# Performance work log

Measured on AMD Instinct MI355X. Metric: run time of the kernel, lower is better.

The kernel has to match this reference:

```python
import jax, jax.numpy as jnp
import numpy as np
import math

B, S, D = 16, 512, 1024
H, L = 16, 4
DH = D // H
EPS = 1e-5


def _layernorm(x, w, b):
    mu = jnp.mean(x, axis=-1, keepdims=True)
    var = jnp.mean(jnp.square(x - mu), axis=-1, keepdims=True)
    return (x - mu) / jnp.sqrt(var + EPS) * w + b


def _pos_encoding(s, d):
    pos = jnp.arange(s, dtype=jnp.float32)[:, None]                      # [s,1]
    div = jnp.exp(jnp.arange(0, d, 2, dtype=jnp.float32) * (-math.log(10000.0) / d))
    ang = pos * div[None, :]                                             # [s,d/2]
    return jnp.stack([jnp.sin(ang), jnp.cos(ang)], axis=-1).reshape(s, d)  # interleave sin/cos


def _attention_layer(x, Wq, bq, Wv, bv, Wo, bo, gamma, ln_w, ln_b, mask):
    bs, s, d = x.shape
    # q_linear == k_linear (kq_same=True)
    q = (x @ Wq.T + bq).reshape(bs, s, H, DH).transpose(0, 2, 1, 3)      # [b,h,s,dh]
    k = q
    v = (x @ Wv.T + bv).reshape(bs, s, H, DH).transpose(0, 2, 1, 3)

    scores = jnp.einsum('bhqd,bhkd->bhqk', q, k) / math.sqrt(DH)         # [b,h,s,s]

    # distance-decay modulation (dist_scores is detached in the original)
    p = jax.nn.softmax(jnp.where(mask, scores, -1e32), axis=-1)
    distcum = jnp.cumsum(p, axis=-1)
    disttot = jnp.sum(p, axis=-1, keepdims=True)
    idx = jnp.arange(s, dtype=jnp.float32)
    pos_eff = jnp.abs(idx[None, :] - idx[:, None])[None, None, :, :]     # |i-j|
    dist = jnp.sqrt(jnp.maximum((disttot - distcum) * pos_eff, 0.0))
    dist = jax.lax.stop_gradient(dist)

    g = -jnp.abs(gamma)[None, :, None, None]                             # [1,h,1,1]
    total_effect = jnp.clip(jnp.exp(dist * g), 1e-5, 1e5)
    scores = scores * total_effect

    scores = jnp.where(mask, scores, -1e32)
    attn = jax.nn.softmax(scores, axis=-1)
    attn = jnp.where(mask, attn, 0.0)

    # maxout=True (peek_cur=False): clamp(1/max, max=5)
    scale = jnp.minimum(1.0 / jnp.max(attn, axis=-1, keepdims=True), 5.0)
    attn = attn * scale

    out = jnp.einsum('bhqk,bhkd->bhqd', attn, v)                         # [b,h,s,dh]
    out = out.transpose(0, 2, 1, 3).reshape(bs, s, d)
    out = out @ Wo.T + bo

    # eval mode: dropout = identity; residual + layernorm
    return _layernorm(x + out, ln_w, ln_b), attn


def reference(x, lens, Wq, bq, Wv, bv, Wo, bo, gammas, ln_w, ln_b, fln_w, fln_b):
    del lens  # only used in training-mode random masking
    s = x.shape[1]
    q = x + _pos_encoding(s, D)[None, :, :]
    mask = jnp.tril(jnp.ones((s, s), dtype=bool), -1)[None, None, :, :]  # peek_cur=False
    scores = None
    for l in range(L):
        q, scores = _attention_layer(q, Wq[l], bq[l], Wv[l], bv[l], Wo[l], bo[l],
                                     gammas[l], ln_w[l], ln_b[l], mask)
    return _layernorm(q, fln_w, fln_b), scores


def setup_inputs() -> dict:
    key = jax.random.key(0)
    ks = jax.random.split(key, 8)
    wscale = 1.0 / math.sqrt(D)
    return {
        'x': jax.random.normal(ks[0], (B, S, D), dtype=jnp.float32),
        'lens': jax.random.randint(ks[1], (B,), 1, S),
        'Wq': jax.random.normal(ks[2], (L, D, D), dtype=jnp.float32) * wscale,
        'bq': jnp.zeros((L, D), dtype=jnp.float32),
        'Wv': jax.random.normal(ks[3], (L, D, D), dtype=jnp.float32) * wscale,
        'bv': jnp.zeros((L, D), dtype=jnp.float32),
        'Wo': jax.random.normal(ks[4], (L, D, D), dtype=jnp.float32) * wscale,
        'bo': jnp.zeros((L, D), dtype=jnp.float32),
        'gammas': jax.random.uniform(ks[5], (L, H), dtype=jnp.float32, minval=-1.7, maxval=1.7),
        'ln_w': jnp.ones((L, D), dtype=jnp.float32),
        'ln_b': jnp.zeros((L, D), dtype=jnp.float32),
        'fln_w': jnp.ones((D,), dtype=jnp.float32),
        'fln_b': jnp.zeros((D,), dtype=jnp.float32),
    }
```

## Files before the change

### kernel.cpp

```cpp
#include <hip/hip_runtime.h>
#include <hip/hip_bf16.h>

#define BB 16
#define SS 512
#define DD 1024
#define HH 16
#define LL 4
#define DHH 64
#define GK 1024

typedef __attribute__((ext_vector_type(8))) short short8;
typedef __attribute__((ext_vector_type(4))) float f32x4;
typedef __attribute__((ext_vector_type(8))) _Float16 half8;

__device__ __forceinline__ unsigned short f2bf(float f) {
  union { float f; unsigned int u; } v; v.f = f;
  unsigned int r = v.u + 0x7FFFu + ((v.u >> 16) & 1u);
  return (unsigned short)(r >> 16);
}
__device__ __forceinline__ float bf2f(unsigned short u) {
  union { unsigned int i; float f; } v; v.i = ((unsigned)u) << 16; return v.f;
}

__device__ __forceinline__ float wave_max(float v) {
#pragma unroll
  for (int off = 32; off > 0; off >>= 1) v = fmaxf(v, __shfl_xor(v, off));
  return v;
}
__device__ __forceinline__ float wave_sum(float v) {
#pragma unroll
  for (int off = 32; off > 0; off >>= 1) v += __shfl_xor(v, off);
  return v;
}
__device__ __forceinline__ float half_max(float v) {
#pragma unroll
  for (int off = 16; off > 0; off >>= 1) v = fmaxf(v, __shfl_xor(v, off));
  return v;
}
__device__ __forceinline__ float half_sum(float v) {
#pragma unroll
  for (int off = 16; off > 0; off >>= 1) v += __shfl_xor(v, off);
  return v;
}

__device__ __forceinline__ void gl16(const void* g, void* l) {
  __builtin_amdgcn_global_load_lds(
      (const __attribute__((address_space(1))) unsigned int*)(uintptr_t)g,
      (__attribute__((address_space(3))) unsigned int*)(unsigned int)(uintptr_t)l,
      16, 0, 0);
}

__global__ __launch_bounds__(256) void k_w2bf_all(
    const float* __restrict__ wq, const float* __restrict__ wv,
    const float* __restrict__ wo, unsigned short* __restrict__ oqv,
    unsigned short* __restrict__ oo) {
  size_t i4 = ((size_t)blockIdx.x * 256 + threadIdx.x) * 4;
  const size_t QV = (size_t)2 * LL * DD * DD;
  const float* src;
  unsigned short* dst;
  if (i4 < QV) {
    size_t l = i4 >> 21;
    size_t r = i4 & ((1u << 21) - 1);
    src = (r < (1u << 20)) ? wq + (l << 20) + r
                           : wv + (l << 20) + (r - (1u << 20));
    dst = oqv + i4;
  } else {
    size_t j = i4 - QV;
    src = wo + j;
    dst = oo + j;
  }
  float4 v = *(const float4*)src;
  uint2 pk;
  pk.x = (unsigned)f2bf(v.x) | ((unsigned)f2bf(v.y) << 16);
  pk.y = (unsigned)f2bf(v.z) | ((unsigned)f2bf(v.w) << 16);
  *(uint2*)dst = pk;
}

__global__ __launch_bounds__(256) void k_add_pe(const float* __restrict__ x,
                                                unsigned short* __restrict__ outb) {
  size_t i4 = ((size_t)blockIdx.x * 256 + threadIdx.x) * 4;
  int d0 = (int)(i4 & (DD - 1));
  int s = (int)((i4 >> 10) & (SS - 1));
  float4 xv = *(const float4*)(x + i4);
  int ip0 = d0 >> 1;
  float f0 = __expf((float)ip0 * -0.017988946039016f);
  float f1 = __expf((float)(ip0 + 1) * -0.017988946039016f);
  float s0v, c0v, s1v, c1v;
  __sincosf((float)s * f0, &s0v, &c0v);
  __sincosf((float)s * f1, &s1v, &c1v);
  float o0 = xv.x + s0v, o1 = xv.y + c0v, o2 = xv.z + s1v, o3 = xv.w + c1v;
  uint2 pk;
  pk.x = (unsigned)f2bf(o0) | ((unsigned)f2bf(o1) << 16);
  pk.y = (unsigned)f2bf(o2) | ((unsigned)f2bf(o3) << 16);
  *(uint2*)(outb + i4) = pk;
}

template <int MODE>
__global__ __launch_bounds__(256) void k_gemm(
    const unsigned short* __restrict__ A, const unsigned short* __restrict__ W,
    const float* __restrict__ bias, const float* __restrict__ bias2,
    void* __restrict__ out, void* __restrict__ out2) {
  __shared__ unsigned short As[2][128 * 32];
  __shared__ unsigned short Bs[2][128 * 32];
  const int tid = threadIdx.x;
  const int lane = tid & 63;
  const int w = tid >> 6;
  const int wr = w >> 1, wc = w & 1;
  const int fr = lane & 15, fq = lane >> 4;

  int bid = blockIdx.x;
  const int cpx = gridDim.x >> 3;
  bid = (bid & 7) * cpx + (bid >> 3);
  const int bm = (bid & 63) * 128;
  const int bn = (bid >> 6) * 128;

  f32x4 acc[4][4] = {};

  const unsigned short* ga = A + (size_t)(bm + w * 16 + (lane >> 2)) * GK + (lane & 3) * 8;
  const unsigned short* gb = W + (size_t)(bn + w * 16 + (lane >> 2)) * GK + (lane & 3) * 8;

  auto STAGE = [&](int buf, int k0) {
    unsigned short* la = As[buf] + w * 512;
    unsigned short* lb = Bs[buf] + w * 512;
    gl16(ga + k0, la);
    gl16(ga + 64 * GK + k0, la + 2048);
    gl16(gb + k0, lb);
    gl16(gb + 64 * GK + k0, lb + 2048);
  };

  STAGE(0, 0);
  __syncthreads();
  int cur = 0;
  for (int k0 = 0; k0 < GK; k0 += 32) {
    if (k0 + 32 < GK) STAGE(cur ^ 1, k0 + 32);
    short8 af[4], bf[4];
#pragma unroll
    for (int m = 0; m < 4; ++m)
      af[m] = *(const short8*)(As[cur] + (wr * 64 + m * 16 + fr) * 32 + fq * 8);
#pragma unroll
    for (int n = 0; n < 4; ++n)
      bf[n] = *(const short8*)(Bs[cur] + (wc * 64 + n * 16 + fr) * 32 + fq * 8);
#pragma unroll
    for (int m = 0; m < 4; ++m)
#pragma unroll
      for (int n = 0; n < 4; ++n)
        acc[m][n] = __builtin_amdgcn_mfma_f32_16x16x32_bf16(af[m], bf[n], acc[m][n], 0, 0, 0);
    __syncthreads();
    cur ^= 1;
  }

#pragma unroll
  for (int m = 0; m < 4; ++m) {
    const int row0 = bm + wr * 64 + m * 16 + fq * 4;
#pragma unroll
    for (int n = 0; n < 4; ++n) {
      const int col = bn + wc * 64 + n * 16 + fr;
      if constexpr (MODE == 0) {
        const float bsv = bias[col];
        unsigned short* o = (unsigned short*)out;
#pragma unroll
        for (int r = 0; r < 4; ++r)
          o[(size_t)(row0 + r) * DD + col] = f2bf(acc[m][n][r] + bsv);
      } else {
        if (col < DD) {
          const float bsv = bias[col];
          unsigned short* o = (unsigned short*)out;
#pragma unroll
          for (int r = 0; r < 4; ++r)
            o[(size_t)(row0 + r) * DD + col] = f2bf(acc[m][n][r] + bsv);
        } else {
          const int c2 = col - DD;
          const float bsv = bias2[c2];
          unsigned short* o = (unsigned short*)out2;
          const int bi = row0 >> 9, si = row0 & (SS - 1);
          uint2 pk;
          pk.x = (unsigned)f2bf(acc[m][n][0] + bsv) | ((unsigned)f2bf(acc[m][n][1] + bsv) << 16);
          pk.y = (unsigned)f2bf(acc[m][n][2] + bsv) | ((unsigned)f2bf(acc[m][n][3] + bsv) << 16);
          *(uint2*)(o + ((size_t)bi * DD + c2) * SS + si) = pk;
        }
      }
    }
  }
}

__global__ __launch_bounds__(512) void k_attn(
    const unsigned short* __restrict__ Q, const unsigned short* __restrict__ Vt,
    const float* __restrict__ gam, unsigned short* __restrict__ AO,
    float* __restrict__ scores_out) {
  __shared__ _Float16 sc_s[64][520];
  __shared__ unsigned short KV[64][72];

  const int tid = threadIdx.x;
  const int lane = tid & 63;
  const int w = tid >> 6;
  const int wr = w & 3;
  const int wc = w >> 2;
  const int fr = lane & 15, fq = lane >> 4;

  const int itile = 7 - (blockIdx.x >> 8);
  const int bh = blockIdx.x & 255;
  const int b = bh >> 4;
  const int h = bh & 15;
  const int i0 = itile * 64;
  const int njt = itile + 1;
  const int jcap = njt * 64;

  const unsigned short* Qb = Q + (size_t)b * SS * DD + h * DHH;
  const unsigned short* Vtb = Vt + ((size_t)b * DD + h * DHH) * SS;
  const float gneg = -fabsf(gam[h]);

  const int srow = tid >> 3;
  const int sdb = (tid & 7) * 8;

  const unsigned short* qrow = Qb + (size_t)(i0 + wr * 16 + fr) * DD;
  short8 a0 = *(const short8*)(qrow + fq * 8);
  short8 a1 = *(const short8*)(qrow + 32 + fq * 8);

  short8 kreg = *(const short8*)(Qb + (size_t)srow * DD + sdb);
  for (int jt = 0; jt < njt; ++jt) {
    *(short8*)&KV[srow][sdb] = kreg;
    const unsigned short* nsrc = (jt + 1 < njt)
        ? Qb + (size_t)((jt + 1) * 64 + srow) * DD + sdb
        : Vtb + (size_t)srow * SS + sdb;
    kreg = *(const short8*)nsrc;
    __syncthreads();

    short8 b00 = *(const short8*)&KV[wc * 32 + fr][fq * 8];
    short8 b01 = *(const short8*)&KV[wc * 32 + fr][32 + fq * 8];
    short8 b10 = *(const short8*)&KV[wc * 32 + 16 + fr][fq * 8];
    short8 b11 = *(const short8*)&KV[wc * 32 + 16 + fr][32 + fq * 8];
    f32x4 s0 = {}, s1 = {};
    __builtin_amdgcn_s_setprio(1);
    s0 = __builtin_amdgcn_mfma_f32_16x16x32_bf16(a0, b00, s0, 0, 0, 0);
    s0 = __builtin_amdgcn_mfma_f32_16x16x32_bf16(a1, b01, s0, 0, 0, 0);
    s1 = __builtin_amdgcn_mfma_f32_16x16x32_bf16(a0, b10, s1, 0, 0, 0);
    s1 = __builtin_amdgcn_mfma_f32_16x16x32_bf16(a1, b11, s1, 0, 0, 0);
    __builtin_amdgcn_s_setprio(0);

#pragma unroll
    for (int n = 0; n < 2; ++n) {
      const int j = jt * 64 + wc * 32 + n * 16 + fr;
#pragma unroll
      for (int r = 0; r < 4; ++r) {
        const int row = wr * 16 + fq * 4 + r;
        const float val = (n ? s1[r] : s0[r]) * 0.125f;
        sc_s[row][j] = (j < i0 + row) ? (_Float16)val : (_Float16)(-65504.0f);
      }
    }
    __syncthreads();
  }
  *(short8*)&KV[srow][sdb] = kreg;

  if (itile >= 4) {
    const int jb = lane << 3;
#pragma unroll 2
    for (int q = 0; q < 8; ++q) {
      const int r_i = w * 8 + q;
      const int gi = i0 + r_i;
      half8 hv = *(const half8*)(&sc_s[r_i][0] + jb);
      float sc[8];
#pragma unroll
      for (int c = 0; c < 8; ++c) sc[c] = (float)hv[c];
#pragma unroll
      for (int c = 0; c < 8; ++c)
        if (jb + c >= jcap) sc[c] = -1e30f;

      float p[8];
      float lsum = 0.0f;
#pragma unroll
      for (int c = 0; c < 8; ++c) {
        p[c] = __expf(sc[c]);
        lsum += p[c];
      }

      float xs = lsum;
#pragma unroll
      for (int off = 1; off < 64; off <<= 1) {
        float y = __shfl_up(xs, off);
        if (lane >= off) xs += y;
      }
      const float tot = __shfl(xs, 63);
      const float inv = 1.0f / tot;
      float run = xs - lsum;

      float s2[8];
      float m2l = -3e38f;
#pragma unroll
      for (int c = 0; c < 8; ++c) {
        run += p[c];
        float cum = run * inv;
        float dist = sqrtf(fmaxf((1.0f - cum) * (float)(gi - (jb + c)), 0.0f));
        float te = __expf(gneg * dist);
        te = fminf(fmaxf(te, 1e-5f), 1e5f);
        s2[c] = sc[c] * te;
        m2l = fmaxf(m2l, s2[c]);
      }
      float e[8];
      float ls2 = 0.0f;
#pragma unroll
      for (int c = 0; c < 8; ++c) {
        e[c] = __expf(s2[c]);
        ls2 += e[c];
      }
      const float m2 = wave_max(m2l);
      const float tot2 = wave_sum(ls2);
      const float rr = tot2 * __expf(-m2);
      const float mult = fminf(rr, 5.0f) / tot2;

      float av[8];
#pragma unroll
      for (int c = 0; c < 8; ++c) av[c] = (gi == 0) ? 0.0f : e[c] * mult;

      if (scores_out) {
        float* so = scores_out + ((size_t)(b * HH + h) * SS + gi) * SS + jb;
        *(float4*)(so) = make_float4(av[0], av[1], av[2], av[3]);
        *(float4*)(so + 4) = make_float4(av[4], av[5], av[6], av[7]);
      }

      short8 pk;
#pragma unroll
      for (int c = 0; c < 8; ++c) pk[c] = (short)f2bf(av[c]);
      *(short8*)((unsigned short*)&sc_s[r_i][0] + jb) = pk;
    }
  } else {
    const int half = lane >> 5;
    const int ll = lane & 31;
    const int jb = ll << 3;
    for (int q = 0; q < 4; ++q) {
      const int r_i = w * 8 + q * 2 + half;
      const int gi = i0 + r_i;
      half8 hv = *(const half8*)(&sc_s[r_i][0] + jb);
      float sc[8];
#pragma unroll
      for (int c = 0; c < 8; ++c) sc[c] = (float)hv[c];
#pragma unroll
      for (int c = 0; c < 8; ++c)
        if (jb + c >= jcap) sc[c] = -1e30f;

      float p[8];
      float lsum = 0.0f;
#pragma unroll
      for (int c = 0; c < 8; ++c) {
        p[c] = __expf(sc[c]);
        lsum += p[c];
      }

      float xs = lsum;
#pragma unroll
      for (int off = 1; off < 32; off <<= 1) {
        float y = __shfl_up(xs, off, 32);
        if (ll >= off) xs += y;
      }
      const float tot = __shfl(xs, 31, 32);
      const float inv = 1.0f / tot;
      float run = xs - lsum;

      float s2[8];
      float m2l = -3e38f;
#pragma unroll
      for (int c = 0; c < 8; ++c) {
        run += p[c];
        float cum = run * inv;
        float dist = sqrtf(fmaxf((1.0f - cum) * (float)(gi - (jb + c)), 0.0f));
        float te = __expf(gneg * dist);
        te = fminf(fmaxf(te, 1e-5f), 1e5f);
        s2[c] = sc[c] * te;
        m2l = fmaxf(m2l, s2[c]);
      }
      float e[8];
      float ls2 = 0.0f;
#pragma unroll
      for (int c = 0; c < 8; ++c) {
        e[c] = __expf(s2[c]);
        ls2 += e[c];
      }
      const float m2 = half_max(m2l);
      const float tot2 = half_sum(ls2);
      const float rr = tot2 * __expf(-m2);
      const float mult = fminf(rr, 5.0f) / tot2;

      float av[8];
#pragma unroll
      for (int c = 0; c < 8; ++c) av[c] = (gi == 0) ? 0.0f : e[c] * mult;

      if (scores_out) {
        float* so = scores_out + ((size_t)(b * HH + h) * SS + gi) * SS + jb;
        *(float4*)(so) = make_float4(av[0], av[1], av[2], av[3]);
        *(float4*)(so + 4) = make_float4(av[4], av[5], av[6], av[7]);
        *(float4*)(so + 256) = make_float4(0.f, 0.f, 0.f, 0.f);
        *(float4*)(so + 260) = make_float4(0.f, 0.f, 0.f, 0.f);
      }

      short8 pk;
#pragma unroll
      for (int c = 0; c < 8; ++c) pk[c] = (short)f2bf(av[c]);
      *(short8*)((unsigned short*)&sc_s[r_i][0] + jb) = pk;
    }
  }
  __syncthreads();

  short8 vreg;
  if (njt > 1) vreg = *(const short8*)(Vtb + (size_t)srow * SS + 64 + sdb);
  f32x4 o0 = {}, o1 = {};
  for (int jt = 0; jt < njt; ++jt) {
    const unsigned short* arow = (const unsigned short*)&sc_s[wr * 16 + fr][0];
    short8 pa0 = *(const short8*)(arow + jt * 64 + fq * 8);
    short8 pa1 = *(const short8*)(arow + jt * 64 + 32 + fq * 8);
    short8 c00 = *(const short8*)&KV[wc * 32 + fr][fq * 8];
    short8 c01 = *(const short8*)&KV[wc * 32 + fr][32 + fq * 8];
    short8 c10 = *(const short8*)&KV[wc * 32 + 16 + fr][fq * 8];
    short8 c11 = *(const short8*)&KV[wc * 32 + 16 + fr][32 + fq * 8];
    __builtin_amdgcn_s_setprio(1);
    o0 = __builtin_amdgcn_mfma_f32_16x16x32_bf16(pa0, c00, o0, 0, 0, 0);
    o0 = __builtin_amdgcn_mfma_f32_16x16x32_bf16(pa1, c01, o0, 0, 0, 0);
    o1 = __builtin_amdgcn_mfma_f32_16x16x32_bf16(pa0, c10, o1, 0, 0, 0);
    o1 = __builtin_amdgcn_mfma_f32_16x16x32_bf16(pa1, c11, o1, 0, 0, 0);
    __builtin_amdgcn_s_setprio(0);
    __syncthreads();
    if (jt + 1 < njt) {
      *(short8*)&KV[srow][sdb] = vreg;
      if (jt + 2 < njt) vreg = *(const short8*)(Vtb + (size_t)srow * SS + (jt + 2) * 64 + sdb);
      __syncthreads();
    }
  }

#pragma unroll
  for (int n = 0; n < 2; ++n) {
    const int d = h * DHH + wc * 32 + n * 16 + fr;
#pragma unroll
    for (int r = 0; r < 4; ++r) {
      const int row = i0 + wr * 16 + fq * 4 + r;
      AO[((size_t)b * SS + row) * DD + d] = f2bf(n ? o1[r] : o0[r]);
    }
  }
}

__global__ __launch_bounds__(256) void k_res_ln(
    const unsigned short* __restrict__ x, const unsigned short* __restrict__ r,
    const float* __restrict__ w, const float* __restrict__ b,
    unsigned short* __restrict__ outb, float* __restrict__ outf) {
  __shared__ float red[4];
  const int row = blockIdx.x;
  const int tid = threadIdx.x;
  const int lane = tid & 63, wv = tid >> 6;
  uint2 xa = ((const uint2*)(x + (size_t)row * DD))[tid];
  float y0 = bf2f((unsigned short)xa.x);
  float y1 = bf2f((unsigned short)(xa.x >> 16));
  float y2 = bf2f((unsigned short)xa.y);
  float y3 = bf2f((unsigned short)(xa.y >> 16));
  if (r) {
    uint2 ra = ((const uint2*)(r + (size_t)row * DD))[tid];
    y0 += bf2f((unsigned short)ra.x);
    y1 += bf2f((unsigned short)(ra.x >> 16));
    y2 += bf2f((unsigned short)ra.y);
    y3 += bf2f((unsigned short)(ra.y >> 16));
  }
  float s = y0 + y1 + y2 + y3;
  s = wave_sum(s);
  if (lane == 0) red[wv] = s;
  __syncthreads();
  float mean = (red[0] + red[1] + red[2] + red[3]) * (1.0f / DD);
  __syncthreads();
  float d0 = y0 - mean, d1 = y1 - mean, d2 = y2 - mean, d3 = y3 - mean;
  float s2 = d0 * d0 + d1 * d1 + d2 * d2 + d3 * d3;
  s2 = wave_sum(s2);
  if (lane == 0) red[wv] = s2;
  __syncthreads();
  float var = (red[0] + red[1] + red[2] + red[3]) * (1.0f / DD);
  float rstd = rsqrtf(var + 1e-5f);
  float4 ww = ((const float4*)w)[tid];
  float4 bb = ((const float4*)b)[tid];
  float o0 = d0 * rstd * ww.x + bb.x;
  float o1 = d1 * rstd * ww.y + bb.y;
  float o2 = d2 * rstd * ww.z + bb.z;
  float o3 = d3 * rstd * ww.w + bb.w;
  if (outf) {
    ((float4*)(outf + (size_t)row * DD))[tid] = make_float4(o0, o1, o2, o3);
  } else {
    uint2 pk;
    pk.x = (unsigned)f2bf(o0) | ((unsigned)f2bf(o1) << 16);
    pk.y = (unsigned)f2bf(o2) | ((unsigned)f2bf(o3) << 16);
    ((uint2*)(outb + (size_t)row * DD))[tid] = pk;
  }
}

extern "C" void kernel_launch(void* const* d_in, const int* in_sizes, int n_in,
                              void* d_out, int out_size, void* d_ws, size_t ws_size,
                              hipStream_t stream) {
  (void)in_sizes; (void)n_in; (void)out_size; (void)ws_size;
  const float* x = (const float*)d_in[0];
  const float* Wq = (const float*)d_in[2];
  const float* bq = (const float*)d_in[3];
  const float* Wv = (const float*)d_in[4];
  const float* bv = (const float*)d_in[5];
  const float* Wo = (const float*)d_in[6];
  const float* bo = (const float*)d_in[7];
  const float* gam = (const float*)d_in[8];
  const float* lnw = (const float*)d_in[9];
  const float* lnb = (const float*)d_in[10];
  const float* flnw = (const float*)d_in[11];
  const float* flnb = (const float*)d_in[12];

  float* out0 = (float*)d_out;
  float* scores = out0 + (size_t)BB * SS * DD;
  const size_t BUF = (size_t)BB * SS * DD;
  const size_t WSZ = (size_t)LL * DD * DD;
  const size_t BHSS = (size_t)BB * HH * SS * SS;

  unsigned short* us = (unsigned short*)d_ws;
  unsigned short* Abf0 = us;
  unsigned short* Abf1 = us + BUF;
  unsigned short* Qbf = us + 2 * BUF;
  unsigned short* VtB = us + 3 * BUF;
  unsigned short* AObf = us + 4 * BUF;
  unsigned short* Pb = us + 5 * BUF;
  unsigned short* Wob = us + 6 * BUF;
  unsigned short* Wqvb = (unsigned short*)scores + (2 * BHSS - 2 * WSZ);

  const int M = BB * SS;

  k_w2bf_all<<<dim3(3 * WSZ / 1024), 256, 0, stream>>>(Wq, Wv, Wo, Wqvb, Wob);
  k_add_pe<<<dim3(BUF / 1024), 256, 0, stream>>>(x, Abf0);

  unsigned short* Acur = Abf0;
  unsigned short* Anx = Abf1;
  for (int l = 0; l < LL; ++l) {
    float* sc_dst = (l == LL - 1) ? scores : nullptr;
    k_gemm<3><<<dim3(1024), 256, 0, stream>>>(Acur, Wqvb + (size_t)l * 2048 * DD,
                                              bq + l * DD, bv + l * DD, Qbf, VtB);
    k_attn<<<dim3(BB * HH * 8), 512, 0, stream>>>(Qbf, VtB, gam + l * HH, AObf, sc_dst);
    k_gemm<0><<<dim3(512), 256, 0, stream>>>(AObf, Wob + (size_t)l * DD * DD,
                                             bo + l * DD, nullptr, Pb, nullptr);
    k_res_ln<<<dim3(M), 256, 0, stream>>>(Acur, Pb, lnw + l * DD, lnb + l * DD, Anx, nullptr);
    unsigned short* t = Acur; Acur = Anx; Anx = t;
  }
  k_res_ln<<<dim3(M), 256, 0, stream>>>(Acur, nullptr, flnw, flnb, nullptr, out0);
}
```

Before: 781.4 us.

## Load V fragments directly from global memory in PV loop, drop LDS staging

The attention kernel's P·V loop now reads each wave's V-transposed MFMA fragments straight from global memory, register double-buffered one tile ahead. This removes the LDS staging of V and the two barriers per tile. The GEMM kernel's block-index swizzle is also replaced with a fixed XCD-aware mapping for computing bm. In exchange, the two waves that share a V tile each load it separately, adding redundant global/L2 traffic and more register pressure.

```diff
diff --git a/kernel.cpp b/kernel.cpp
--- a/kernel.cpp
+++ b/kernel.cpp
@@ -108,10 +108,8 @@
   const int wr = w >> 1, wc = w & 1;
   const int fr = lane & 15, fq = lane >> 4;
 
-  int bid = blockIdx.x;
-  const int cpx = gridDim.x >> 3;
-  bid = (bid & 7) * cpx + (bid >> 3);
-  const int bm = (bid & 63) * 128;
+  const int bid = blockIdx.x;
+  const int bm = ((bid & 7) * 8 + ((bid >> 3) & 7)) * 128;
   const int bn = (bid >> 6) * 128;
 
   f32x4 acc[4][4] = {};
@@ -219,10 +217,8 @@
   short8 kreg = *(const short8*)(Qb + (size_t)srow * DD + sdb);
   for (int jt = 0; jt < njt; ++jt) {
     *(short8*)&KV[srow][sdb] = kreg;
-    const unsigned short* nsrc = (jt + 1 < njt)
-        ? Qb + (size_t)((jt + 1) * 64 + srow) * DD + sdb
-        : Vtb + (size_t)srow * SS + sdb;
-    kreg = *(const short8*)nsrc;
+    if (jt + 1 < njt)
+      kreg = *(const short8*)(Qb + (size_t)((jt + 1) * 64 + srow) * DD + sdb);
     __syncthreads();
 
     short8 b00 = *(const short8*)&KV[wc * 32 + fr][fq * 8];
@@ -249,7 +245,6 @@
     }
     __syncthreads();
   }
-  *(short8*)&KV[srow][sdb] = kreg;
 
   if (itile >= 4) {
     const int jb = lane << 3;
@@ -399,29 +394,32 @@
   }
   __syncthreads();
 
-  short8 vreg;
-  if (njt > 1) vreg = *(const short8*)(Vtb + (size_t)srow * SS + 64 + sdb);
+  const unsigned short* vb0 = Vtb + (size_t)(wc * 32 + fr) * SS;
+  const unsigned short* vb1 = Vtb + (size_t)(wc * 32 + 16 + fr) * SS;
+  short8 c00 = *(const short8*)(vb0 + fq * 8);
+  short8 c01 = *(const short8*)(vb0 + 32 + fq * 8);
+  short8 c10 = *(const short8*)(vb1 + fq * 8);
+  short8 c11 = *(const short8*)(vb1 + 32 + fq * 8);
   f32x4 o0 = {}, o1 = {};
   for (int jt = 0; jt < njt; ++jt) {
+    short8 n00 = c00, n01 = c01, n10 = c10, n11 = c11;
+    if (jt + 1 < njt) {
+      const int off = (jt + 1) * 64;
+      n00 = *(const short8*)(vb0 + off + fq * 8);
+      n01 = *(const short8*)(vb0 + off + 32 + fq * 8);
+      n10 = *(const short8*)(vb1 + off + fq * 8);
+      n11 = *(const short8*)(vb1 + off + 32 + fq * 8);
+    }
     const unsigned short* arow = (const unsigned short*)&sc_s[wr * 16 + fr][0];
     short8 pa0 = *(const short8*)(arow + jt * 64 + fq * 8);
     short8 pa1 = *(const short8*)(arow + jt * 64 + 32 + fq * 8);
-    short8 c00 = *(const short8*)&KV[wc * 32 + fr][fq * 8];
-    short8 c01 = *(const short8*)&KV[wc * 32 + fr][32 + fq * 8];
-    short8 c10 = *(const short8*)&KV[wc * 32 + 16 + fr][fq * 8];
-    short8 c11 = *(const short8*)&KV[wc * 32 + 16 + fr][32 + fq * 8];
     __builtin_amdgcn_s_setprio(1);
     o0 = __builtin_amdgcn_mfma_f32_16x16x32_bf16(pa0, c00, o0, 0, 0, 0);
     o0 = __builtin_amdgcn_mfma_f32_16x16x32_bf16(pa1, c01, o0, 0, 0, 0);
     o1 = __builtin_amdgcn_mfma_f32_16x16x32_bf16(pa0, c10, o1, 0, 0, 0);
     o1 = __builtin_amdgcn_mfma_f32_16x16x32_bf16(pa1, c11, o1, 0, 0, 0);
     __builtin_amdgcn_s_setprio(0);
-    __syncthreads();
-    if (jt + 1 < njt) {
-      *(short8*)&KV[srow][sdb] = vreg;
-      if (jt + 2 < njt) vreg = *(const short8*)(Vtb + (size_t)srow * SS + (jt + 2) * 64 + sdb);
-      __syncthreads();
-    }
+    c00 = n00; c01 = n01; c10 = n10; c11 = n11;
   }
 
 #pragma unroll
```

Measured after the change: 758.2 us. 1.03x faster.
